# Kernel tuning notes

Hardware: AMD Instinct MI355X
Metric: run time of the kernel (lower is better)

## Reference

```python
import jax, jax.numpy as jnp
import numpy as np

EMBED = 512
HEADS = 8
HEAD_DIM = EMBED // HEADS


def setup_inputs() -> dict:
    key = jax.random.key(0)
    ks = jax.random.split(key, 9)
    N, L = 4, 2048
    values = jax.random.normal(ks[0], (N, L, EMBED), dtype=jnp.float32)
    keys = jax.random.normal(ks[1], (N, L, EMBED), dtype=jnp.float32)
    query = jax.random.normal(ks[2], (N, L, EMBED), dtype=jnp.float32)
    mask = jax.random.randint(ks[3], (N, 1, 1, L), 0, 2, dtype=jnp.int32)
    s_h = 1.0 / np.sqrt(HEAD_DIM).astype(np.float32)
    s_e = 1.0 / np.sqrt(EMBED).astype(np.float32)
    Wv = jax.random.normal(ks[4], (HEAD_DIM, HEAD_DIM), dtype=jnp.float32) * s_h
    Wk = jax.random.normal(ks[5], (HEAD_DIM, HEAD_DIM), dtype=jnp.float32) * s_h
    Wq = jax.random.normal(ks[6], (HEAD_DIM, HEAD_DIM), dtype=jnp.float32) * s_h
    Wo = jax.random.normal(ks[7], (EMBED, EMBED), dtype=jnp.float32) * s_e
    bo = jnp.zeros((EMBED,), dtype=jnp.float32)
    return {"values": values, "keys": keys, "query": query, "mask": mask,
            "Wv": Wv, "Wk": Wk, "Wq": Wq, "Wo": Wo, "bo": bo}


def reference(values, keys, query, mask, Wv, Wk, Wq, Wo, bo):
    N, Lq, E = query.shape
    D = Wv.shape[0]
    H = E // D
    Lk = keys.shape[1]
    # split heads: [N, L, H, D]
    v = values.reshape(N, values.shape[1], H, D)
    k = keys.reshape(N, Lk, H, D)
    q = query.reshape(N, Lq, H, D)
    # per-head linear projections (nn.Linear: x @ W^T, no bias)
    v = jnp.einsum("nlhd,ed->nlhe", v, Wv)
    k = jnp.einsum("nlhd,ed->nlhe", k, Wk)
    q = jnp.einsum("nlhd,ed->nlhe", q, Wq)
    # energy: [N, H, Lq, Lk]
    energy = jnp.einsum("nqhd,nkhd->nhqk", q, k)
    energy = jnp.where(mask == 0, jnp.float32(-1e20), energy)
    # NOTE: original scales by sqrt(embed_size), not sqrt(head_dim)
    attn = jax.nn.softmax(energy / jnp.sqrt(jnp.float32(E)), axis=3)
    out = jnp.einsum("nhqk,nkhd->nqhd", attn, v).reshape(N, Lq, E)
    return out @ Wo.T + bo
```

## Files before the change

### kernel.cpp

```cpp
#include <hip/hip_runtime.h>

#define LSEQ 2048
#define EMB  512
#define NH   8
#define HD   64
#define NBATCH 4
#define QSCALE (0.044194173824159216f * 1.4426950408889634f)

using short8  = __attribute__((ext_vector_type(8))) short;
using short4v = __attribute__((ext_vector_type(4))) short;
using f32x4   = __attribute__((ext_vector_type(4))) float;

__device__ __forceinline__ short bf16r(float f) {
  union { float f; unsigned u; } x; x.f = f;
  unsigned r = x.u + 0x7FFFu + ((x.u >> 16) & 1u);
  return (short)(r >> 16);
}

__device__ __forceinline__ float exp2v(float x) {
  float r;
  asm("v_exp_f32 %0, %1" : "=v"(r) : "v"(x));
  return r;
}

__device__ __forceinline__ unsigned cvtpk(float lo, float hi) {
  unsigned r;
  asm("v_cvt_pk_bf16_f32 %0, %1, %2" : "=v"(r) : "v"(lo), "v"(hi));
  return r;
}

__device__ __forceinline__ void stage16(const void* g, void* l) {
  __builtin_amdgcn_global_load_lds(
      (const __attribute__((address_space(1))) unsigned int*)g,
      (__attribute__((address_space(3))) unsigned int*)l, 16, 0, 0);
}

__device__ __forceinline__ short8 cvt8(const float* __restrict__ p) {
  float4 a = ((const float4*)p)[0];
  float4 b = ((const float4*)p)[1];
  short8 r;
  r[0]=bf16r(a.x); r[1]=bf16r(a.y); r[2]=bf16r(a.z); r[3]=bf16r(a.w);
  r[4]=bf16r(b.x); r[5]=bf16r(b.y); r[6]=bf16r(b.z); r[7]=bf16r(b.w);
  return r;
}

__device__ __forceinline__ short8 ld8(const short* __restrict__ p) {
  return *(const short8*)p;
}

__global__ __launch_bounds__(256) void prep_kernel(
    const float* __restrict__ Wo, short* __restrict__ Wob,
    const int* __restrict__ mask, float* __restrict__ fbias,
    int* __restrict__ kidx, int* __restrict__ meta,
    const float* __restrict__ Wq, const float* __restrict__ Wk,
    const float* __restrict__ Wv, short* __restrict__ Wqb,
    short* __restrict__ Wkb, short* __restrict__ Wvb) {
  __shared__ int ssum[256];
  int b = blockIdx.x;
  int tid = threadIdx.x;
  if (b < 256) {
    int i = b * 256 + tid;
    float4 v = ((const float4*)Wo)[i];
    short4v r;
    r[0]=bf16r(v.x); r[1]=bf16r(v.y); r[2]=bf16r(v.z); r[3]=bf16r(v.w);
    ((short4v*)Wob)[i] = r;
  } else if (b < 260) {
    int n = b - 256;
    int base = n * LSEQ;
    int loc[8], c = 0;
#pragma unroll
    for (int j = 0; j < 8; j++) { loc[j] = mask[base + tid * 8 + j] != 0; c += loc[j]; }
    ssum[tid] = c;
    __syncthreads();
    for (int off = 1; off < 256; off <<= 1) {
      int v = (tid >= off) ? ssum[tid - off] : 0;
      __syncthreads();
      ssum[tid] += v;
      __syncthreads();
    }
    int total = ssum[255];
    int excl = ssum[tid] - c;
    int qz = (total == 0);
#pragma unroll
    for (int j = 0; j < 8; j++) {
      int i = tid * 8 + j;
      kidx[base + i] = qz ? i : 0;
      fbias[base + i] = (qz || i < total) ? 0.f : -1e30f;
    }
    __syncthreads();
    if (!qz) {
      int pos = excl;
#pragma unroll
      for (int j = 0; j < 8; j++)
        if (loc[j]) { kidx[base + pos] = tid * 8 + j; pos++; }
    }
    if (tid == 0) {
      meta[n] = qz ? (LSEQ / 64) : ((total + 63) >> 6);
      meta[4 + n] = qz;
    }
  } else {
    int t = (b - 260) >> 2;
    int i = ((b - 260) & 3) * 256 + tid;
    const float* W = (t == 0) ? Wq : (t == 1) ? Wk : Wv;
    short* O = (t == 0) ? Wqb : (t == 1) ? Wkb : Wvb;
    float sc = (t == 0) ? QSCALE : 1.f;
    float4 v = ((const float4*)W)[i];
    short4v r;
    r[0]=bf16r(v.x*sc); r[1]=bf16r(v.y*sc); r[2]=bf16r(v.z*sc); r[3]=bf16r(v.w*sc);
    ((short4v*)O)[i] = r;
  }
}

__global__ __launch_bounds__(256) void proj_kernel(
    const float* __restrict__ query, const float* __restrict__ keys,
    const float* __restrict__ values,
    const short* __restrict__ Wqb, const short* __restrict__ Wkb,
    const short* __restrict__ Wvb, const int* __restrict__ kidx,
    const int* __restrict__ meta,
    short* __restrict__ Qp, short* __restrict__ Kp, short* __restrict__ Vt) {
  __shared__ short tile[64][72];
  int t = blockIdx.y;
  const float* x = (t == 0) ? query : (t == 1) ? keys : values;
  const short* W = (t == 0) ? Wqb   : (t == 1) ? Wkb  : Wvb;
  int idx = blockIdx.x;
  int lt = idx & 31, h = (idx >> 5) & 7, n = idx >> 8;
  int tid = threadIdx.x, lane = tid & 63, w = tid >> 6;
  int row16 = lane & 15, g = lane >> 4;
  int lbase = lt * 64 + w * 16;

  int zq = 0;
  const float* xr;
  int lrow = lbase + row16;
  if (t == 0) {
    zq = meta[4 + n];
    xr = x + ((size_t)(n * LSEQ + lrow)) * EMB + h * HD + g * 8;
  } else {
    if (lbase >= ((meta[n] + 1) & ~1) * 64) return;
    int gidx = kidx[n * LSEQ + lrow];
    xr = x + ((size_t)(n * LSEQ + gidx)) * EMB + h * HD + g * 8;
  }
  short8 a0 = cvt8(xr);
  short8 a1 = cvt8(xr + 32);

  f32x4 acc[4];
#pragma unroll
  for (int et = 0; et < 4; et++) acc[et] = (f32x4){0.f, 0.f, 0.f, 0.f};
#pragma unroll
  for (int et = 0; et < 4; et++) {
    const short* wr = W + (size_t)(et * 16 + row16) * HD + g * 8;
    short8 b0 = ld8(wr);
    short8 b1 = ld8(wr + 32);
    acc[et] = __builtin_amdgcn_mfma_f32_16x16x32_bf16(a0, b0, acc[et], 0, 0, 0);
    acc[et] = __builtin_amdgcn_mfma_f32_16x16x32_bf16(a1, b1, acc[et], 0, 0, 0);
  }
  if (zq) {
#pragma unroll
    for (int et = 0; et < 4; et++) acc[et] = (f32x4){0.f, 0.f, 0.f, 0.f};
  }

  if (t == 2) {
#pragma unroll
    for (int et = 0; et < 4; et++)
#pragma unroll
      for (int r = 0; r < 4; r++)
        tile[et * 16 + row16][w * 16 + g * 4 + r] = bf16r(acc[et][r]);
  } else {
#pragma unroll
    for (int et = 0; et < 4; et++)
#pragma unroll
      for (int r = 0; r < 4; r++)
        tile[w * 16 + g * 4 + r][et * 16 + row16] = bf16r(acc[et][r]);
  }
  __syncthreads();

  size_t nh = (size_t)(n * NH + h);
#pragma unroll
  for (int i = tid; i < 512; i += 256) {
    int rr = i >> 3, cc = i & 7;
    short8 v = *(const short8*)&tile[rr][cc * 8];
    if (t == 2)
      *(short8*)(Vt + (nh * HD + rr) * LSEQ + lt * 64 + cc * 8) = v;
    else {
      short* O = (t == 0) ? Qp : Kp;
      *(short8*)(O + (nh * LSEQ + lt * 64 + rr) * HD + cc * 8) = v;
    }
  }
}

__global__ __launch_bounds__(256, 2) void attn_kernel(
    const short* __restrict__ Qp, const short* __restrict__ Kp,
    const short* __restrict__ Vt, const float* __restrict__ fbias,
    const int* __restrict__ meta, short* __restrict__ aout) {
  __shared__ __align__(16) char smem[81920];

  int idx = blockIdx.x;
  int h = idx & 7;
  int qt = (idx >> 3) & 15;
  int n = idx >> 7;
  int tid = threadIdx.x, lane = tid & 63, w = tid >> 6;
  int q0 = lane & 15, g = lane >> 4;
  int xr = q0 & 7;
  int nkt = (meta[n] + 1) >> 1;

  size_t nh = (size_t)(n * NH + h);
  const short* Qb = Qp + (nh * LSEQ + qt * 128 + w * 32) * HD;
  short8 bq00 = ld8(Qb + q0 * HD + g * 8);
  short8 bq01 = ld8(Qb + q0 * HD + 32 + g * 8);
  short8 bq10 = ld8(Qb + (16 + q0) * HD + g * 8);
  short8 bq11 = ld8(Qb + (16 + q0) * HD + 32 + g * 8);

  f32x4 acc0[4], acc1[4];
#pragma unroll
  for (int dt = 0; dt < 4; dt++) {
    acc0[dt] = (f32x4){0.f, 0.f, 0.f, 0.f};
    acc1[dt] = (f32x4){0.f, 0.f, 0.f, 0.f};
  }
  float l0 = 0.f, l1 = 0.f;

  const char* Ksrc = (const char*)(Kp + nh * (size_t)LSEQ * HD);
  const char* Vsrc = (const char*)(Vt + nh * (size_t)HD * LSEQ);
  const float* fb  = fbias + n * LSEQ + g * 4;

  int ksoff[4], vsoff[4], ldo[4];
#pragma unroll
  for (int j = 0; j < 4; j++) {
    int c = j * 256 + w * 64 + lane;
    int rK = c >> 3, cwK = (c & 7) ^ (rK & 7);
    ksoff[j] = rK * 128 + cwK * 16;
    int rV = c >> 4, cwV = c & 15;
    int sub = (cwV & 7) ^ (rV & 7);
    vsoff[j] = rV * (LSEQ * 2) + ((cwV & 8) + sub) * 16;
    ldo[j] = (j * 256 + w * 64) * 16;
  }

  int kfragb = q0 * 128 + ((g ^ xr) << 4);
  int vfragb = q0 * 256 + ((g ^ xr) << 4);
  int pbase = 65536 + w * 4096 + q0 * 128;
  char* pw_[4];
#pragma unroll
  for (int ks = 0; ks < 4; ks++)
    pw_[ks] = smem + pbase + ((ks * 32 + g * 8) ^ (xr << 4));
  const char* pr0 = smem + pbase + ((g * 16) ^ (xr << 4));
  const char* pr1 = smem + pbase + ((64 + g * 16) ^ (xr << 4));

#pragma unroll
  for (int j = 0; j < 4; j++) stage16(Ksrc + ksoff[j], smem + ldo[j]);
#pragma unroll
  for (int j = 0; j < 4; j++) stage16(Vsrc + vsoff[j], smem + 32768 + ldo[j]);
  __syncthreads();

  for (int kt = 0; kt < nkt; kt++) {
    int buf = kt & 1;
    if (kt < nkt - 1) {
      int bo = (buf ^ 1) * 16384;
      const char* Kn = Ksrc + (size_t)(kt + 1) * (128 * 128);
      const char* Vn = Vsrc + (size_t)(kt + 1) * 256;
#pragma unroll
      for (int j = 0; j < 4; j++) stage16(Kn + ksoff[j], smem + bo + ldo[j]);
#pragma unroll
      for (int j = 0; j < 4; j++) stage16(Vn + vsoff[j], smem + 32768 + bo + ldo[j]);
    }

#pragma unroll
    for (int h2 = 0; h2 < 2; h2++) {
      f32x4 fbv[4];
#pragma unroll
      for (int ks = 0; ks < 4; ks++)
        fbv[ks] = *(const f32x4*)(fb + kt * 128 + h2 * 64 + ks * 16);

      int kb_l = buf * 16384 + h2 * 8192 + kfragb;
      f32x4 s0[4], s1[4];
      __builtin_amdgcn_s_setprio(1);
#pragma unroll
      for (int ks = 0; ks < 4; ks++) {
        short8 k0 = *(const short8*)(smem + (kb_l + ks * 2048));
        short8 k1 = *(const short8*)(smem + ((kb_l + ks * 2048) ^ 64));
        f32x4 t0 = __builtin_amdgcn_mfma_f32_16x16x32_bf16(k0, bq00, fbv[ks], 0, 0, 0);
        s0[ks]   = __builtin_amdgcn_mfma_f32_16x16x32_bf16(k1, bq01, t0, 0, 0, 0);
        f32x4 t1 = __builtin_amdgcn_mfma_f32_16x16x32_bf16(k0, bq10, fbv[ks], 0, 0, 0);
        s1[ks]   = __builtin_amdgcn_mfma_f32_16x16x32_bf16(k1, bq11, t1, 0, 0, 0);
      }
      __builtin_amdgcn_s_setprio(0);

      float ps0 = 0.f, ps1 = 0.f;
#pragma unroll
      for (int ks = 0; ks < 4; ks++) {
        float p0 = exp2v(s0[ks][0] - 32.f), p1 = exp2v(s0[ks][1] - 32.f);
        float p2 = exp2v(s0[ks][2] - 32.f), p3 = exp2v(s0[ks][3] - 32.f);
        ps0 += (p0 + p1) + (p2 + p3);
        *(int2*)pw_[ks] = make_int2((int)cvtpk(p0, p1), (int)cvtpk(p2, p3));
        float q1 = exp2v(s1[ks][0] - 32.f), q2 = exp2v(s1[ks][1] - 32.f);
        float q3 = exp2v(s1[ks][2] - 32.f), q4 = exp2v(s1[ks][3] - 32.f);
        ps1 += (q1 + q2) + (q3 + q4);
        *(int2*)(pw_[ks] + 2048) = make_int2((int)cvtpk(q1, q2), (int)cvtpk(q3, q4));
      }
      l0 += ps0; l1 += ps1;

      asm volatile("s_waitcnt lgkmcnt(0)" ::: "memory");

      short8 ap00 = *(const short8*)pr0;
      short8 ap01 = *(const short8*)pr1;
      short8 ap10 = *(const short8*)(pr0 + 2048);
      short8 ap11 = *(const short8*)(pr1 + 2048);
      int vb_l = 32768 + buf * 16384 + vfragb + h2 * 128;
      __builtin_amdgcn_s_setprio(1);
#pragma unroll
      for (int dt = 0; dt < 4; dt++) {
        short8 v0 = *(const short8*)(smem + (vb_l + dt * 4096));
        short8 v1 = *(const short8*)(smem + ((vb_l + dt * 4096) ^ 64));
        acc0[dt] = __builtin_amdgcn_mfma_f32_16x16x32_bf16(ap00, v0, acc0[dt], 0, 0, 0);
        acc0[dt] = __builtin_amdgcn_mfma_f32_16x16x32_bf16(ap01, v1, acc0[dt], 0, 0, 0);
        acc1[dt] = __builtin_amdgcn_mfma_f32_16x16x32_bf16(ap10, v0, acc1[dt], 0, 0, 0);
        acc1[dt] = __builtin_amdgcn_mfma_f32_16x16x32_bf16(ap11, v1, acc1[dt], 0, 0, 0);
      }
      __builtin_amdgcn_s_setprio(0);
    }

    __syncthreads();
  }

  l0 += __shfl_xor(l0, 16);  l0 += __shfl_xor(l0, 32);
  l1 += __shfl_xor(l1, 16);  l1 += __shfl_xor(l1, 32);
  float li0 = l0 > 0.f ? 1.f / l0 : 0.f;
  float li1 = l1 > 0.f ? 1.f / l1 : 0.f;
  int lb = lane & 48;
  float w0[4], w1[4];
#pragma unroll
  for (int r = 0; r < 4; r++) {
    w0[r] = __shfl(li0, lb + g * 4 + r);
    w1[r] = __shfl(li1, lb + g * 4 + r);
  }
  int qrow = qt * 128 + w * 32;
#pragma unroll
  for (int r = 0; r < 4; r++) {
    size_t o0 = ((size_t)(n * LSEQ + qrow + g * 4 + r)) * EMB + h * HD;
    size_t o1 = ((size_t)(n * LSEQ + qrow + 16 + g * 4 + r)) * EMB + h * HD;
#pragma unroll
    for (int dt = 0; dt < 4; dt++) {
      aout[o0 + dt * 16 + q0] = bf16r(acc0[dt][r] * w0[r]);
      aout[o1 + dt * 16 + q0] = bf16r(acc1[dt][r] * w1[r]);
    }
  }
}

__global__ __launch_bounds__(256) void outproj_kernel(
    const short* __restrict__ aout, const short* __restrict__ Wob,
    const float* __restrict__ bo, float* __restrict__ out) {
  int mt = blockIdx.x, nt = blockIdx.y;
  int tid = threadIdx.x, lane = tid & 63, w = tid >> 6;
  int row16 = lane & 15, g = lane >> 4;
  int mrow = mt * 128 + w * 32;

  f32x4 acc0[4], acc1[4];
#pragma unroll
  for (int et = 0; et < 4; et++) {
    acc0[et] = (f32x4){0.f, 0.f, 0.f, 0.f};
    acc1[et] = (f32x4){0.f, 0.f, 0.f, 0.f};
  }

  for (int kc = 0; kc < 16; kc++) {
    short8 a0 = ld8(aout + (size_t)(mrow + row16) * EMB + kc * 32 + g * 8);
    short8 a1 = ld8(aout + (size_t)(mrow + 16 + row16) * EMB + kc * 32 + g * 8);
#pragma unroll
    for (int et = 0; et < 4; et++) {
      short8 b = ld8(Wob + (size_t)(nt * 64 + et * 16 + row16) * EMB + kc * 32 + g * 8);
      acc0[et] = __builtin_amdgcn_mfma_f32_16x16x32_bf16(a0, b, acc0[et], 0, 0, 0);
      acc1[et] = __builtin_amdgcn_mfma_f32_16x16x32_bf16(a1, b, acc1[et], 0, 0, 0);
    }
  }
#pragma unroll
  for (int et = 0; et < 4; et++) {
    int e = nt * 64 + et * 16 + row16;
    float bias = bo[e];
#pragma unroll
    for (int r = 0; r < 4; r++) {
      out[(size_t)(mrow + g * 4 + r) * EMB + e] = acc0[et][r] + bias;
      out[(size_t)(mrow + 16 + g * 4 + r) * EMB + e] = acc1[et][r] + bias;
    }
  }
}

extern "C" void kernel_launch(void* const* d_in, const int* in_sizes, int n_in,
                              void* d_out, int out_size, void* d_ws, size_t ws_size,
                              hipStream_t stream) {
  const float* values = (const float*)d_in[0];
  const float* keys   = (const float*)d_in[1];
  const float* query  = (const float*)d_in[2];
  const int*   mask   = (const int*)d_in[3];
  const float* Wv     = (const float*)d_in[4];
  const float* Wk     = (const float*)d_in[5];
  const float* Wq     = (const float*)d_in[6];
  const float* Wo     = (const float*)d_in[7];
  const float* bo     = (const float*)d_in[8];
  float* out = (float*)d_out;

  short* Qp = (short*)d_out;
  short* Kp = (short*)((char*)d_out + (8u << 20));
  char* ws = (char*)d_ws;
  short* Vt    = (short*)(ws);
  short* aout  = (short*)(ws + (8u << 20));
  short* Wob   = (short*)(ws + (16u << 20));
  float* fbias = (float*)(ws + (16u << 20) + (512u << 10));
  int*   kidx  = (int*)  (ws + (16u << 20) + (544u << 10));
  int*   meta  = (int*)  (ws + (16u << 20) + (576u << 10));
  short* Wqb   = (short*)(ws + (16u << 20) + (577u << 10));
  short* Wkb   = (short*)(ws + (16u << 20) + (585u << 10));
  short* Wvb   = (short*)(ws + (16u << 20) + (593u << 10));

  prep_kernel<<<272, 256, 0, stream>>>(Wo, Wob, mask, fbias, kidx, meta,
                                       Wq, Wk, Wv, Wqb, Wkb, Wvb);
  proj_kernel<<<dim3(NBATCH * NH * (LSEQ / 64), 3), 256, 0, stream>>>(
      query, keys, values, Wqb, Wkb, Wvb, kidx, meta, Qp, Kp, Vt);
  attn_kernel<<<NBATCH * NH * (LSEQ / 128), 256, 0, stream>>>(
      Qp, Kp, Vt, fbias, meta, aout);
  outproj_kernel<<<dim3((NBATCH * LSEQ) / 128, EMB / 64), 256, 0, stream>>>(
      aout, Wob, bo, out);
}
```

Measured before the change: 84.63 us.

## Move Wo conversion into attention tail blocks and enlarge outproj M tile

Result: no change. 83.56 us (-1.3%).

```diff
diff --git a/kernel.cpp b/kernel.cpp
--- a/kernel.cpp
+++ b/kernel.cpp
@@ -49,7 +49,6 @@
 }
 
 __global__ __launch_bounds__(256) void prep_kernel(
-    const float* __restrict__ Wo, short* __restrict__ Wob,
     const int* __restrict__ mask, float* __restrict__ fbias,
     int* __restrict__ kidx, int* __restrict__ meta,
     const float* __restrict__ Wq, const float* __restrict__ Wk,
@@ -58,14 +57,8 @@
   __shared__ int ssum[256];
   int b = blockIdx.x;
   int tid = threadIdx.x;
-  if (b < 256) {
-    int i = b * 256 + tid;
-    float4 v = ((const float4*)Wo)[i];
-    short4v r;
-    r[0]=bf16r(v.x); r[1]=bf16r(v.y); r[2]=bf16r(v.z); r[3]=bf16r(v.w);
-    ((short4v*)Wob)[i] = r;
-  } else if (b < 260) {
-    int n = b - 256;
+  if (b < 4) {
+    int n = b;
     int base = n * LSEQ;
     int loc[8], c = 0;
 #pragma unroll
@@ -99,8 +92,8 @@
       meta[4 + n] = qz;
     }
   } else {
-    int t = (b - 260) >> 2;
-    int i = ((b - 260) & 3) * 256 + tid;
+    int t = (b - 4) >> 2;
+    int i = ((b - 4) & 3) * 256 + tid;
     const float* W = (t == 0) ? Wq : (t == 1) ? Wk : Wv;
     short* O = (t == 0) ? Wqb : (t == 1) ? Wkb : Wvb;
     float sc = (t == 0) ? QSCALE : 1.f;
@@ -190,14 +183,24 @@
 __global__ __launch_bounds__(256, 2) void attn_kernel(
     const short* __restrict__ Qp, const short* __restrict__ Kp,
     const short* __restrict__ Vt, const float* __restrict__ fbias,
-    const int* __restrict__ meta, short* __restrict__ aout) {
+    const int* __restrict__ meta, short* __restrict__ aout,
+    const float* __restrict__ Wo, short* __restrict__ Wob) {
   __shared__ __align__(16) char smem[81920];
 
   int idx = blockIdx.x;
+  int tid = threadIdx.x;
+  if (idx >= NBATCH * NH * (LSEQ / 128)) {
+    int i = (idx - NBATCH * NH * (LSEQ / 128)) * 256 + tid;
+    float4 v = ((const float4*)Wo)[i];
+    short4v r;
+    r[0]=bf16r(v.x); r[1]=bf16r(v.y); r[2]=bf16r(v.z); r[3]=bf16r(v.w);
+    ((short4v*)Wob)[i] = r;
+    return;
+  }
   int h = idx & 7;
   int qt = (idx >> 3) & 15;
   int n = idx >> 7;
-  int tid = threadIdx.x, lane = tid & 63, w = tid >> 6;
+  int lane = tid & 63, w = tid >> 6;
   int q0 = lane & 15, g = lane >> 4;
   int xr = q0 & 7;
   int nkt = (meta[n] + 1) >> 1;
@@ -349,23 +352,25 @@
   int mt = blockIdx.x, nt = blockIdx.y;
   int tid = threadIdx.x, lane = tid & 63, w = tid >> 6;
   int row16 = lane & 15, g = lane >> 4;
-  int mrow = mt * 128 + w * 32;
-
-  f32x4 acc0[4], acc1[4];
-#pragma unroll
-  for (int et = 0; et < 4; et++) {
-    acc0[et] = (f32x4){0.f, 0.f, 0.f, 0.f};
-    acc1[et] = (f32x4){0.f, 0.f, 0.f, 0.f};
-  }
+  int mrow = mt * 256 + w * 64;
+
+  f32x4 acc[4][4];
+#pragma unroll
+  for (int hh = 0; hh < 4; hh++)
+#pragma unroll
+    for (int et = 0; et < 4; et++) acc[hh][et] = (f32x4){0.f, 0.f, 0.f, 0.f};
 
   for (int kc = 0; kc < 16; kc++) {
-    short8 a0 = ld8(aout + (size_t)(mrow + row16) * EMB + kc * 32 + g * 8);
-    short8 a1 = ld8(aout + (size_t)(mrow + 16 + row16) * EMB + kc * 32 + g * 8);
+    short8 a[4];
+#pragma unroll
+    for (int hh = 0; hh < 4; hh++)
+      a[hh] = ld8(aout + (size_t)(mrow + hh * 16 + row16) * EMB + kc * 32 + g * 8);
 #pragma unroll
     for (int et = 0; et < 4; et++) {
       short8 b = ld8(Wob + (size_t)(nt * 64 + et * 16 + row16) * EMB + kc * 32 + g * 8);
-      acc0[et] = __builtin_amdgcn_mfma_f32_16x16x32_bf16(a0, b, acc0[et], 0, 0, 0);
-      acc1[et] = __builtin_amdgcn_mfma_f32_16x16x32_bf16(a1, b, acc1[et], 0, 0, 0);
+#pragma unroll
+      for (int hh = 0; hh < 4; hh++)
+        acc[hh][et] = __builtin_amdgcn_mfma_f32_16x16x32_bf16(a[hh], b, acc[hh][et], 0, 0, 0);
     }
   }
 #pragma unroll
@@ -373,10 +378,10 @@
     int e = nt * 64 + et * 16 + row16;
     float bias = bo[e];
 #pragma unroll
-    for (int r = 0; r < 4; r++) {
-      out[(size_t)(mrow + g * 4 + r) * EMB + e] = acc0[et][r] + bias;
-      out[(size_t)(mrow + 16 + g * 4 + r) * EMB + e] = acc1[et][r] + bias;
-    }
+    for (int hh = 0; hh < 4; hh++)
+#pragma unroll
+      for (int r = 0; r < 4; r++)
+        out[(size_t)(mrow + hh * 16 + g * 4 + r) * EMB + e] = acc[hh][et][r] + bias;
   }
 }
 
@@ -407,12 +412,12 @@
   short* Wkb   = (short*)(ws + (16u << 20) + (585u << 10));
   short* Wvb   = (short*)(ws + (16u << 20) + (593u << 10));
 
-  prep_kernel<<<272, 256, 0, stream>>>(Wo, Wob, mask, fbias, kidx, meta,
-                                       Wq, Wk, Wv, Wqb, Wkb, Wvb);
+  prep_kernel<<<16, 256, 0, stream>>>(mask, fbias, kidx, meta,
+                                      Wq, Wk, Wv, Wqb, Wkb, Wvb);
   proj_kernel<<<dim3(NBATCH * NH * (LSEQ / 64), 3), 256, 0, stream>>>(
       query, keys, values, Wqb, Wkb, Wvb, kidx, meta, Qp, Kp, Vt);
-  attn_kernel<<<NBATCH * NH * (LSEQ / 128), 256, 0, stream>>>(
-      Qp, Kp, Vt, fbias, meta, aout);
-  outproj_kernel<<<dim3((NBATCH * LSEQ) / 128, EMB / 64), 256, 0, stream>>>(
+  attn_kernel<<<NBATCH * NH * (LSEQ / 128) + 256, 256, 0, stream>>>(
+      Qp, Kp, Vt, fbias, meta, aout, Wo, Wob);
+  outproj_kernel<<<dim3((NBATCH * LSEQ) / 256, EMB / 64), 256, 0, stream>>>(
       aout, Wob, bo, out);
 }
```
